# Performance work log

Measured on AMD Instinct MI355X. Metric: run time of the kernel, lower is better.

Reference implementation:

```python
import jax, jax.numpy as jnp
from jax import lax
import numpy as np

N_FFT = 256
HOP = 128
NUM_EXPERTS = 8
TOPK = 2
B = 128
L = 4096


def conv1d(x, w, b, pad):
    # x [N,C,T], w [O,I,K]
    y = lax.conv_general_dilated(x, w, (1,), [(pad, pad)],
                                 dimension_numbers=('NCH', 'OIH', 'NCH'))
    return y + b[None, :, None]


def maxpool1d(x, p):
    return lax.reduce_window(x, -jnp.inf, lax.max, (1, 1, p), (1, 1, p), 'VALID')


def se_block(x, w1, w2):
    # x [B,C,T]; squeeze-excitation with no-bias linears
    y = x.mean(-1)
    y = jax.nn.relu(y @ w1.T)
    y = jax.nn.sigmoid(y @ w2.T)
    return x * y[:, :, None]


def interp_linear(x, out_len):
    # F.interpolate(mode='linear', align_corners=False) on [B,C,T]
    Lin = x.shape[-1]
    scale = Lin / out_len
    coords = jnp.clip((jnp.arange(out_len, dtype=x.dtype) + 0.5) * scale - 0.5, 0.0, Lin - 1)
    lo = jnp.floor(coords).astype(jnp.int32)
    hi = jnp.minimum(lo + 1, Lin - 1)
    w = (coords - lo).astype(x.dtype)
    return x[..., lo] * (1.0 - w) + x[..., hi] * w


def lstm_scan(x, wih, whh, bih, bhh):
    # x [T,B,D] -> hidden seq [T,B,H]; torch gate order i,f,g,o
    H = whh.shape[1]
    def step(carry, xt):
        h, c = carry
        gates = xt @ wih.T + h @ whh.T + bih + bhh
        i, f, g, o = jnp.split(gates, 4, axis=-1)
        c = jax.nn.sigmoid(f) * c + jax.nn.sigmoid(i) * jnp.tanh(g)
        h = jax.nn.sigmoid(o) * jnp.tanh(c)
        return (h, c), h
    z = jnp.zeros((x.shape[1], H), x.dtype)
    _, hs = lax.scan(step, (z, z), x)
    return hs


def _forward(x_continuum, x_normalized,
             gate_w1, gate_b1, gate_w2, gate_b2,
             exp_w1, exp_b1, exp_w2, exp_b2,
             lw1, lb1, lw2, lb2, se2_w1, se2_w2, lw3, lb3, se3_w1, se3_w2,
             wih_f, whh_f, bih_f, bhh_f, wih_b, whh_b, bih_b, bhh_b,
             ffn_w1, ffn_b1, ffn_w2, ffn_b2):
    Bsz = x_continuum.shape[0]
    # --- STFT magnitude (center=True, reflect pad, periodic hann window) ---
    n = jnp.arange(N_FFT, dtype=x_continuum.dtype)
    win = 0.5 * (1.0 - jnp.cos(2.0 * jnp.pi * n / N_FFT))
    xp = jnp.pad(x_continuum, ((0, 0), (N_FFT // 2, N_FFT // 2)), mode='reflect')
    n_frames = 1 + (xp.shape[1] - N_FFT) // HOP  # 33
    idx = jnp.arange(n_frames)[:, None] * HOP + jnp.arange(N_FFT)[None, :]
    frames = xp[:, idx] * win                      # [B,T,N_FFT]
    mag = jnp.abs(jnp.fft.rfft(frames, axis=-1)).transpose(0, 2, 1)  # [B,129,T]
    mag = mag.astype(x_continuum.dtype)
    # --- gating: mean-pool over time, MLP, top-k, softmax over top-k ---
    pooled = mag.mean(-1)                          # [B,129]
    logits = jax.nn.relu(pooled @ gate_w1.T + gate_b1) @ gate_w2.T + gate_b2
    topv, topi = lax.top_k(logits, TOPK)
    gw = jax.nn.softmax(topv, axis=1)              # [B,K]
    # --- dense all-expert conv pyramids (matches original dense compute) ---
    def expert(w1, b1, w2, b2):
        h = jax.nn.relu(conv1d(mag, w1, b1, 2))
        return jax.nn.relu(conv1d(h, w2, b2, 1))
    eo = jax.vmap(expert)(exp_w1, exp_b1, exp_w2, exp_b2)  # [E,B,C,T]
    sel = eo[topi, jnp.arange(Bsz)[:, None]]               # [B,K,C,T]
    freq_feat = jnp.einsum('bk,bkct->bct', gw, sel)        # [B,256,33]
    # --- line attention branch ---
    h = jax.nn.relu(conv1d(x_normalized[:, None, :], lw1, lb1, 3))
    h = maxpool1d(h, 4)
    h = jax.nn.relu(conv1d(h, lw2, lb2, 2))
    h = se_block(h, se2_w1, se2_w2)
    h = maxpool1d(h, 4)
    h = jax.nn.relu(conv1d(h, lw3, lb3, 1))
    h = se_block(h, se3_w1, se3_w2)
    line_feat = maxpool1d(h, 4)                            # [B,256,64]
    # --- length alignment via linear interpolation ---
    t = min(freq_feat.shape[-1], line_feat.shape[-1])
    freq_feat = interp_linear(freq_feat, t)
    line_feat = interp_linear(line_feat, t)
    comb = jnp.concatenate([freq_feat, line_feat], axis=1).transpose(2, 0, 1)  # [T,B,512]
    # --- single-layer bidirectional LSTM, take last time step ---
    hf = lstm_scan(comb, wih_f, whh_f, bih_f, bhh_f)
    hb = lstm_scan(comb[::-1], wih_b, whh_b, bih_b, bhh_b)[::-1]
    last = jnp.concatenate([hf[-1], hb[-1]], axis=-1)      # [B,512]
    # --- prediction head (dropout inactive at inference) ---
    h = jax.nn.relu(last @ ffn_w1.T + ffn_b1)
    return h @ ffn_w2.T + ffn_b2                           # [B,1]


def setup_inputs() -> dict:
    key = jax.random.key(0)
    ks = jax.random.split(key, 40)
    def rn(k, shape, s=0.05):
        return jax.random.normal(k, shape, dtype=jnp.float32) * s
    d = {
        'x_continuum': jax.random.normal(ks[0], (B, L), jnp.float32),
        'x_normalized': jax.random.normal(ks[1], (B, L), jnp.float32),
        'gate_w1': rn(ks[2], (128, 129)), 'gate_b1': rn(ks[3], (128,)),
        'gate_w2': rn(ks[4], (NUM_EXPERTS, 128)), 'gate_b2': rn(ks[5], (NUM_EXPERTS,)),
        'exp_w1': rn(ks[6], (NUM_EXPERTS, 256, 129, 5)), 'exp_b1': rn(ks[7], (NUM_EXPERTS, 256)),
        'exp_w2': rn(ks[8], (NUM_EXPERTS, 256, 256, 3)), 'exp_b2': rn(ks[9], (NUM_EXPERTS, 256)),
        'lw1': rn(ks[10], (64, 1, 7)), 'lb1': rn(ks[11], (64,)),
        'lw2': rn(ks[12], (128, 64, 5)), 'lb2': rn(ks[13], (128,)),
        'se2_w1': rn(ks[14], (32, 128)), 'se2_w2': rn(ks[15], (128, 32)),
        'lw3': rn(ks[16], (256, 128, 3)), 'lb3': rn(ks[17], (256,)),
        'se3_w1': rn(ks[18], (64, 256)), 'se3_w2': rn(ks[19], (256, 64)),
        'wih_f': rn(ks[20], (1024, 512)), 'whh_f': rn(ks[21], (1024, 256)),
        'bih_f': rn(ks[22], (1024,)), 'bhh_f': rn(ks[23], (1024,)),
        'wih_b': rn(ks[24], (1024, 512)), 'whh_b': rn(ks[25], (1024, 256)),
        'bih_b': rn(ks[26], (1024,)), 'bhh_b': rn(ks[27], (1024,)),
        'ffn_w1': rn(ks[28], (256, 512)), 'ffn_b1': rn(ks[29], (256,)),
        'ffn_w2': rn(ks[30], (1, 256)), 'ffn_b2': rn(ks[31], (1,)),
    }
    return d


def reference(x_continuum, x_normalized,
              gate_w1, gate_b1, gate_w2, gate_b2,
              exp_w1, exp_b1, exp_w2, exp_b2,
              lw1, lb1, lw2, lb2, se2_w1, se2_w2, lw3, lb3, se3_w1, se3_w2,
              wih_f, whh_f, bih_f, bhh_f, wih_b, whh_b, bih_b, bhh_b,
              ffn_w1, ffn_b1, ffn_w2, ffn_b2):
    return _forward(x_continuum, x_normalized,
                    gate_w1, gate_b1, gate_w2, gate_b2,
                    exp_w1, exp_b1, exp_w2, exp_b2,
                    lw1, lb1, lw2, lb2, se2_w1, se2_w2, lw3, lb3, se3_w1, se3_w2,
                    wih_f, whh_f, bih_f, bhh_f, wih_b, whh_b, bih_b, bhh_b,
                    ffn_w1, ffn_b1, ffn_w2, ffn_b2)
```

## Files before the change

kernel.cpp:

```cpp
#include <hip/hip_runtime.h>
#include <math.h>

namespace {
constexpr int B = 128;
constexpr int L = 4096;
constexpr int NBIN = 129;
constexpr int NFR = 33;

constexpr size_t F_MAG    = 0;
constexpr size_t F_GW     = F_MAG + 544896;
constexpr size_t F_TOPI   = F_GW + 256;
constexpr size_t F_EH1    = F_TOPI + 256;
constexpr size_t F_SEL    = F_EH1 + 2162688;
constexpr size_t F_LINEF  = F_SEL + 2162688;
constexpr size_t F_COMB   = F_LINEF + 2097152;
constexpr size_t F_XPROJ  = F_COMB + 2162688;
constexpr size_t F_GATESB = F_XPROJ + 4325376;
constexpr size_t F_HF     = F_GATESB + 131072;
constexpr size_t F_HBLAST = F_HF + 32768;
constexpr size_t F_SESUM2 = F_HBLAST + 32768;
constexpr size_t F_SESC2  = F_SESUM2 + 16384;
constexpr size_t F_SESUM3 = F_SESC2 + 16384;
constexpr size_t F_SESC3  = F_SESUM3 + 32768;
constexpr size_t F_WHHB   = F_SESC3 + 32768;
constexpr size_t F_WKB    = F_WHHB + 131072;
constexpr size_t F_WKB3   = F_WKB + 20480;
constexpr size_t F_WIHF   = F_WKB3 + 49152;
constexpr size_t F_WIHB   = F_WIHF + 262144;
constexpr size_t F_BIGA   = F_WIHB + 262144;
constexpr size_t F_BIGB   = F_BIGA + 8388608;
}

typedef __attribute__((ext_vector_type(8))) short bf16x8;
typedef __attribute__((ext_vector_type(4))) float f32x4;

__device__ __forceinline__ float sigm(float x) { return 1.0f / (1.0f + expf(-x)); }

__device__ __forceinline__ float fsigm(float x) { return 1.0f / (1.0f + __expf(-x)); }
__device__ __forceinline__ float ftanh(float x) { return 1.0f - 2.0f / (__expf(2.0f * x) + 1.0f); }

__device__ __forceinline__ unsigned int f2bf_rne(float f) {
    unsigned int u = __float_as_uint(f);
    return (u + 0x7FFFu + ((u >> 16) & 1u)) >> 16;
}

__device__ __forceinline__ float bflo(unsigned int u) { return __uint_as_float(u << 16); }
__device__ __forceinline__ float bfhi(unsigned int u) { return __uint_as_float(u & 0xFFFF0000u); }

__global__ __launch_bounds__(256) void stft_kernel(const float* __restrict__ x,
                                                   float* __restrict__ mag)
{
    int bf = blockIdx.x;
    int b = bf / NFR, f = bf % NFR;
    int tid = threadIdx.x;
    __shared__ float tbl[256];
    __shared__ float fx[256];
    tbl[tid] = cosf(6.28318530717958647692f * (float)tid / 256.0f);
    __syncthreads();
    {
        int j = f * 128 + tid - 128;
        if (j < 0) j = -j;
        else if (j >= L) j = 2 * L - 2 - j;
        float win = 0.5f * (1.0f - tbl[tid]);
        fx[tid] = x[(size_t)b * L + j] * win;
    }
    __syncthreads();
    if (tid < NBIN) {
        float re = 0.f, im = 0.f;
        int m = 0;
        for (int n = 0; n < 256; ++n) {
            float v = fx[n];
            re += v * tbl[m];
            im += v * tbl[(m + 192) & 255];
            m = (m + tid) & 255;
        }
        mag[((size_t)b * NBIN + tid) * NFR + f] = sqrtf(re * re + im * im);
    }
}

__global__ __launch_bounds__(128) void gate_kernel(const float* __restrict__ mag,
                                                   const float* __restrict__ w1,
                                                   const float* __restrict__ b1,
                                                   const float* __restrict__ w2,
                                                   const float* __restrict__ b2,
                                                   int* __restrict__ topi,
                                                   float* __restrict__ gw)
{
    int b = blockIdx.x, tid = threadIdx.x;
    __shared__ float pooled[NBIN];
    __shared__ float h1[128];
    __shared__ float lg[8];
    for (int k = tid; k < NBIN; k += 128) {
        const float* mp = mag + ((size_t)b * NBIN + k) * NFR;
        float s = 0.f;
        for (int f = 0; f < NFR; ++f) s += mp[f];
        pooled[k] = s * (1.0f / 33.0f);
    }
    __syncthreads();
    {
        float acc = b1[tid];
        const float* wr = w1 + tid * NBIN;
        for (int k = 0; k < NBIN; ++k) acc += pooled[k] * wr[k];
        h1[tid] = fmaxf(acc, 0.f);
    }
    __syncthreads();
    if (tid < 8) {
        float a = b2[tid];
        const float* w = w2 + tid * 128;
        for (int j = 0; j < 128; ++j) a += h1[j] * w[j];
        lg[tid] = a;
    }
    __syncthreads();
    if (tid == 0) {
        int i0 = 0; float v0 = lg[0];
        for (int e = 1; e < 8; ++e) if (lg[e] > v0) { v0 = lg[e]; i0 = e; }
        int i1 = -1; float v1 = -3.0e38f;
        for (int e = 0; e < 8; ++e) { if (e == i0) continue; if (lg[e] > v1) { v1 = lg[e]; i1 = e; } }
        float m = fmaxf(v0, v1);
        float e0 = expf(v0 - m), e1 = expf(v1 - m);
        float inv = 1.0f / (e0 + e1);
        topi[b * 2 + 0] = i0; topi[b * 2 + 1] = i1;
        gw[b * 2 + 0] = e0 * inv; gw[b * 2 + 1] = e1 * inv;
    }
}

__global__ __launch_bounds__(512) void expert_conv1_kernel(const float* __restrict__ mag,
                                                           const int* __restrict__ topi,
                                                           const float* __restrict__ W,
                                                           const float* __restrict__ Bb,
                                                           float* __restrict__ out)
{
    int b = blockIdx.x, slot = blockIdx.y;
    int e = topi[b * 2 + slot];
    __shared__ float sm[129 * 37 + 16];
    int tid = threadIdx.x;
    for (int i = tid; i < 129 * 37 + 16; i += 512) sm[i] = 0.f;
    __syncthreads();
    for (int i = tid; i < 129 * 33; i += 512) {
        int ic = i / 33, t = i % 33;
        sm[ic * 37 + 2 + t] = mag[((size_t)b * NBIN + ic) * NFR + t];
    }
    __syncthreads();
    int oc = (blockIdx.z << 7) + (tid >> 2);
    int tq = tid & 3;
    int t0 = tq * 9;
    int nt = (tq == 3) ? 6 : 9;
    float acc[9];
#pragma unroll
    for (int i = 0; i < 9; ++i) acc[i] = 0.f;
    const float* wp = W + ((size_t)e * 256 + oc) * (129 * 5);
    for (int ic = 0; ic < 129; ++ic) {
        const float* wr = wp + ic * 5;
        const float* sr = sm + ic * 37 + t0;
        float w0 = wr[0], w1 = wr[1], w2 = wr[2], w3 = wr[3], w4 = wr[4];
#pragma unroll
        for (int t = 0; t < 9; ++t)
            acc[t] += w0 * sr[t] + w1 * sr[t + 1] + w2 * sr[t + 2] + w3 * sr[t + 3] + w4 * sr[t + 4];
    }
    float bias = Bb[e * 256 + oc];
    float* op = out + (((size_t)b * 2 + slot) * 256 + oc) * NFR + t0;
    for (int t = 0; t < nt; ++t) op[t] = fmaxf(acc[t] + bias, 0.f);
}

__global__ __launch_bounds__(512) void expert_conv2_kernel(const float* __restrict__ eh1,
                                                           const int* __restrict__ topi,
                                                           const float* __restrict__ W,
                                                           const float* __restrict__ Bb,
                                                           float* __restrict__ out)
{
    int b = blockIdx.x, slot = blockIdx.y;
    int e = topi[b * 2 + slot];
    __shared__ float sm[256 * 37 + 16];
    int tid = threadIdx.x;
    for (int i = tid; i < 256 * 37 + 16; i += 512) sm[i] = 0.f;
    __syncthreads();
    for (int i = tid; i < 256 * 33; i += 512) {
        int ic = i / 33, t = i % 33;
        sm[ic * 37 + 2 + t] = eh1[(((size_t)b * 2 + slot) * 256 + ic) * NFR + t];
    }
    __syncthreads();
    int oc = (blockIdx.z << 7) + (tid >> 2);
    int tq = tid & 3;
    int t0 = tq * 9;
    int nt = (tq == 3) ? 6 : 9;
    float acc[9];
#pragma unroll
    for (int i = 0; i < 9; ++i) acc[i] = 0.f;
    const float* wp = W + ((size_t)e * 256 + oc) * (256 * 3);
    for (int ic = 0; ic < 256; ++ic) {
        const float* wr = wp + ic * 3;
        const float* sr = sm + ic * 37 + t0;
        float w0 = wr[0], w1 = wr[1], w2 = wr[2];
#pragma unroll
        for (int t = 0; t < 9; ++t)
            acc[t] += w0 * sr[t + 1] + w1 * sr[t + 2] + w2 * sr[t + 3];
    }
    float bias = Bb[e * 256 + oc];
    float* op = out + (((size_t)b * 2 + slot) * 256 + oc) * NFR + t0;
    for (int t = 0; t < nt; ++t) op[t] = fmaxf(acc[t] + bias, 0.f);
}

__global__ __launch_bounds__(256) void line1_kernel(const float* __restrict__ x,
                                                    const float* __restrict__ lw1,
                                                    const float* __restrict__ lb1,
                                                    unsigned short* __restrict__ p1T)
{
    int b = blockIdx.x;
    int P0 = blockIdx.y * 256;
    __shared__ float sx[1032];
    __shared__ float w[448];
    __shared__ float bb[64];
    __shared__ unsigned short sT[256 * 65];
    int tid = threadIdx.x;
    for (int i = tid; i < 448; i += 256) w[i] = lw1[i];
    for (int i = tid; i < 64; i += 256) bb[i] = lb1[i];
    int base = 4 * P0 - 3;
    for (int i = tid; i < 1032; i += 256) {
        int g = base + i;
        sx[i] = (g >= 0 && g < L) ? x[(size_t)b * L + g] : 0.f;
    }
    __syncthreads();
    int p = tid;
    for (int oc = 0; oc < 64; ++oc) {
        const float* wr = w + oc * 7;
        float best = -3.0e38f;
#pragma unroll
        for (int q = 0; q < 4; ++q) {
            const float* s = sx + 4 * p + q;
            float v = wr[0]*s[0] + wr[1]*s[1] + wr[2]*s[2] + wr[3]*s[3] + wr[4]*s[4] + wr[5]*s[5] + wr[6]*s[6];
            best = fmaxf(best, v);
        }
        float v = fmaxf(best + bb[oc], 0.f);
        sT[p * 65 + oc] = (unsigned short)f2bf_rne(v);
    }
    __syncthreads();
    unsigned int* outw = reinterpret_cast<unsigned int*>(p1T);
    for (int i2 = tid; i2 < 256 * 32; i2 += 256) {
        int row = i2 >> 5, dw = i2 & 31;
        unsigned int lo = sT[row * 65 + dw * 2];
        unsigned int hi = sT[row * 65 + dw * 2 + 1];
        outw[((size_t)b * 1024 + P0 + row) * 32 + dw] = lo | (hi << 16);
    }
}

__global__ __launch_bounds__(256) void prep_wkb_kernel(const float* __restrict__ W,
                                                       unsigned short* __restrict__ wkb)
{
    int idx = blockIdx.x * 256 + threadIdx.x;
    if (idx >= 128 * 320) return;
    int oc = idx / 320, K = idx % 320;
    int k = K >> 6, ic = K & 63;
    wkb[idx] = (unsigned short)f2bf_rne(W[oc * 320 + ic * 5 + k]);
}

__global__ __launch_bounds__(256) void line2_mfma_kernel(const unsigned short* __restrict__ p1T,
                                                         const unsigned short* __restrict__ wkb,
                                                         const float* __restrict__ lb2,
                                                         float* __restrict__ h2,
                                                         float* __restrict__ seSum2)
{
    int b = blockIdx.x;
    int t0 = blockIdx.y * 128;
    __shared__ __align__(16) unsigned short wl[128 * 320];
    __shared__ __align__(16) unsigned short inT[132 * 64];
    __shared__ float bias[128];
    int tid = threadIdx.x;

    for (int idx = tid; idx < 128 * 40; idx += 256) {
        int oc = idx / 40, ch = idx % 40;
        int swz = (ch & ~7) | ((ch & 7) ^ (oc & 7));
        *reinterpret_cast<uint4*>(&wl[oc * 320 + swz * 8]) =
            *reinterpret_cast<const uint4*>(&wkb[oc * 320 + ch * 8]);
    }
    for (int idx = tid; idx < 132 * 8; idx += 256) {
        int j = idx / 8, ch = idx % 8;
        int t = t0 - 2 + j;
        uint4 v = make_uint4(0u, 0u, 0u, 0u);
        if (t >= 0 && t < 1024)
            v = *reinterpret_cast<const uint4*>(&p1T[((size_t)b * 1024 + t) * 64 + ch * 8]);
        int swz = ch ^ (j & 7);
        *reinterpret_cast<uint4*>(&inT[j * 64 + swz * 8]) = v;
    }
    if (tid < 128) bias[tid] = lb2[tid];
    __syncthreads();

    int lane = tid & 63;
    int w = tid >> 6;
    int l15 = lane & 15, g = lane >> 4;

    f32x4 acc[8][2];
#pragma unroll
    for (int ot = 0; ot < 8; ++ot) {
        acc[ot][0] = (f32x4){0.f, 0.f, 0.f, 0.f};
        acc[ot][1] = (f32x4){0.f, 0.f, 0.f, 0.f};
    }

    for (int ks = 0; ks < 10; ++ks) {
        int k = ks >> 1;
        bf16x8 bf0, bf1;
        {
            int j = w * 32 + l15 + k;
            int ch = (ks & 1) * 4 + g;
            bf0 = *reinterpret_cast<const bf16x8*>(&inT[j * 64 + (ch ^ (j & 7)) * 8]);
            int j1 = j + 16;
            bf1 = *reinterpret_cast<const bf16x8*>(&inT[j1 * 64 + (ch ^ (j1 & 7)) * 8]);
        }
#pragma unroll
        for (int ot = 0; ot < 8; ++ot) {
            int row = ot * 16 + l15;
            int ch = ks * 4 + g;
            int swz = (ch & ~7) | ((ch & 7) ^ (row & 7));
            bf16x8 af = *reinterpret_cast<const bf16x8*>(&wl[row * 320 + swz * 8]);
            acc[ot][0] = __builtin_amdgcn_mfma_f32_16x16x32_bf16(af, bf0, acc[ot][0], 0, 0, 0);
            acc[ot][1] = __builtin_amdgcn_mfma_f32_16x16x32_bf16(af, bf1, acc[ot][1], 0, 0, 0);
        }
    }

    int tcol = t0 + w * 32 + l15;
#pragma unroll
    for (int ot = 0; ot < 8; ++ot) {
#pragma unroll
        for (int r = 0; r < 4; ++r) {
            int oc = ot * 16 + g * 4 + r;
            float bv = bias[oc];
            float v0 = fmaxf(acc[ot][0][r] + bv, 0.f);
            float v1 = fmaxf(acc[ot][1][r] + bv, 0.f);
            float* hp = h2 + ((size_t)b * 128 + oc) * 1024 + tcol;
            hp[0] = v0;
            hp[16] = v1;
            float s = v0 + v1;
            s += __shfl_xor(s, 1);
            s += __shfl_xor(s, 2);
            s += __shfl_xor(s, 4);
            s += __shfl_xor(s, 8);
            if (l15 == 0) atomicAdd(&seSum2[b * 128 + oc], s);
        }
    }
}

__global__ __launch_bounds__(128) void se2_kernel(const float* __restrict__ seSum2,
                                                  const float* __restrict__ w1,
                                                  const float* __restrict__ w2,
                                                  float* __restrict__ seScale2)
{
    int b = blockIdx.x, tid = threadIdx.x;
    __shared__ float y[128];
    __shared__ float z[32];
    y[tid] = seSum2[b * 128 + tid] * (1.0f / 1024.0f);
    __syncthreads();
    if (tid < 32) {
        float a = 0.f;
        const float* wr = w1 + tid * 128;
        for (int c = 0; c < 128; ++c) a += y[c] * wr[c];
        z[tid] = fmaxf(a, 0.f);
    }
    __syncthreads();
    {
        float a = 0.f;
        const float* wr = w2 + tid * 32;
        for (int j = 0; j < 32; ++j) a += z[j] * wr[j];
        seScale2[b * 128 + tid] = sigm(a);
    }
}

__global__ __launch_bounds__(256) void pool2t_kernel(const float* __restrict__ h2,
                                                     const float* __restrict__ seScale2,
                                                     unsigned short* __restrict__ p2T)
{
    int b = blockIdx.x, p = threadIdx.x;
    __shared__ unsigned short sT[256 * 129];
    for (int c = 0; c < 128; ++c) {
        float4 v = *reinterpret_cast<const float4*>(&h2[((size_t)b * 128 + c) * 1024 + 4 * p]);
        float m = fmaxf(fmaxf(v.x, v.y), fmaxf(v.z, v.w)) * seScale2[b * 128 + c];
        sT[p * 129 + c] = (unsigned short)f2bf_rne(m);
    }
    __syncthreads();
    unsigned int* out = reinterpret_cast<unsigned int*>(p2T);
    for (int idx = p; idx < 256 * 64; idx += 256) {
        int row = idx >> 6, dw = idx & 63;
        unsigned int lo = sT[row * 129 + dw * 2];
        unsigned int hi = sT[row * 129 + dw * 2 + 1];
        out[((size_t)b * 256 + row) * 64 + dw] = lo | (hi << 16);
    }
}

__global__ __launch_bounds__(256) void prep_wkb3_kernel(const float* __restrict__ W,
                                                        unsigned short* __restrict__ wkb3)
{
    int idx = blockIdx.x * 256 + threadIdx.x;
    if (idx >= 256 * 384) return;
    int oc = idx / 384, K = idx % 384;
    int k = K >> 7, ic = K & 127;
    wkb3[idx] = (unsigned short)f2bf_rne(W[oc * 384 + ic * 3 + k]);
}

__global__ __launch_bounds__(256) void line3_mfma_kernel(const unsigned short* __restrict__ p2T,
                                                         const unsigned short* __restrict__ wkb3,
                                                         const float* __restrict__ lb3,
                                                         float* __restrict__ h3,
                                                         float* __restrict__ seSum3)
{
    int b = blockIdx.x;
    int oc0 = blockIdx.y * 128;
    int t0 = blockIdx.z * 128;
    __shared__ __align__(16) unsigned short wl[128 * 384];
    __shared__ __align__(16) unsigned short inT[130 * 128];
    __shared__ float bias[128];
    int tid = threadIdx.x;

    for (int idx = tid; idx < 128 * 48; idx += 256) {
        int oc = idx / 48, ch = idx % 48;
        int swz = (ch & ~7) | ((ch & 7) ^ (oc & 7));
        *reinterpret_cast<uint4*>(&wl[oc * 384 + swz * 8]) =
            *reinterpret_cast<const uint4*>(&wkb3[(size_t)(oc0 + oc) * 384 + ch * 8]);
    }
    for (int idx = tid; idx < 130 * 16; idx += 256) {
        int j = idx / 16, ch = idx % 16;
        int t = t0 - 1 + j;
        uint4 v = make_uint4(0u, 0u, 0u, 0u);
        if (t >= 0 && t < 256)
            v = *reinterpret_cast<const uint4*>(&p2T[((size_t)b * 256 + t) * 128 + ch * 8]);
        int swz = ch ^ (j & 15);
        *reinterpret_cast<uint4*>(&inT[j * 128 + swz * 8]) = v;
    }
    if (tid < 128) bias[tid] = lb3[oc0 + tid];
    __syncthreads();

    int lane = tid & 63;
    int w = tid >> 6;
    int l15 = lane & 15, g = lane >> 4;

    f32x4 acc[8][2];
#pragma unroll
    for (int ot = 0; ot < 8; ++ot) {
        acc[ot][0] = (f32x4){0.f, 0.f, 0.f, 0.f};
        acc[ot][1] = (f32x4){0.f, 0.f, 0.f, 0.f};
    }

    for (int ks = 0; ks < 12; ++ks) {
        int k = ks >> 2;
        int ch = (ks & 3) * 4 + g;
        bf16x8 bf0, bf1;
        {
            int j = w * 32 + l15 + k;
            bf0 = *reinterpret_cast<const bf16x8*>(&inT[j * 128 + (ch ^ (j & 15)) * 8]);
            int j1 = j + 16;
            bf1 = *reinterpret_cast<const bf16x8*>(&inT[j1 * 128 + (ch ^ (j1 & 15)) * 8]);
        }
#pragma unroll
        for (int ot = 0; ot < 8; ++ot) {
            int row = ot * 16 + l15;
            int wch = ks * 4 + g;
            int swz = (wch & ~7) | ((wch & 7) ^ (row & 7));
            bf16x8 af = *reinterpret_cast<const bf16x8*>(&wl[row * 384 + swz * 8]);
            acc[ot][0] = __builtin_amdgcn_mfma_f32_16x16x32_bf16(af, bf0, acc[ot][0], 0, 0, 0);
            acc[ot][1] = __builtin_amdgcn_mfma_f32_16x16x32_bf16(af, bf1, acc[ot][1], 0, 0, 0);
        }
    }

    int tcol = t0 + w * 32 + l15;
#pragma unroll
    for (int ot = 0; ot < 8; ++ot) {
#pragma unroll
        for (int r = 0; r < 4; ++r) {
            int ocl = ot * 16 + g * 4 + r;
            int oc = oc0 + ocl;
            float bv = bias[ocl];
            float v0 = fmaxf(acc[ot][0][r] + bv, 0.f);
            float v1 = fmaxf(acc[ot][1][r] + bv, 0.f);
            float* hp = h3 + ((size_t)b * 256 + oc) * 256 + tcol;
            hp[0] = v0;
            hp[16] = v1;
            float s = v0 + v1;
            s += __shfl_xor(s, 1);
            s += __shfl_xor(s, 2);
            s += __shfl_xor(s, 4);
            s += __shfl_xor(s, 8);
            if (l15 == 0) atomicAdd(&seSum3[b * 256 + oc], s);
        }
    }
}

__global__ __launch_bounds__(256) void se3_kernel(const float* __restrict__ seSum3,
                                                  const float* __restrict__ w1,
                                                  const float* __restrict__ w2,
                                                  float* __restrict__ seScale3)
{
    int b = blockIdx.x, tid = threadIdx.x;
    __shared__ float y[256];
    __shared__ float z[64];
    y[tid] = seSum3[b * 256 + tid] * (1.0f / 256.0f);
    __syncthreads();
    if (tid < 64) {
        float a = 0.f;
        const float* wr = w1 + tid * 256;
        for (int c = 0; c < 256; ++c) a += y[c] * wr[c];
        z[tid] = fmaxf(a, 0.f);
    }
    __syncthreads();
    {
        float a = 0.f;
        const float* wr = w2 + tid * 64;
        for (int j = 0; j < 64; ++j) a += z[j] * wr[j];
        seScale3[b * 256 + tid] = sigm(a);
    }
}

__global__ __launch_bounds__(256) void pool3_kernel(const float* __restrict__ h3,
                                                    const float* __restrict__ seScale3,
                                                    float* __restrict__ lineFeat)
{
    const int total = 128 * 256 * 64;
    for (int idx = blockIdx.x * 256 + threadIdx.x; idx < total; idx += gridDim.x * 256) {
        int b = idx >> 14;
        int c = (idx >> 6) & 255;
        int p = idx & 63;
        const float* hp = h3 + (((size_t)b * 256 + c) * 256) + 4 * p;
        float v = fmaxf(fmaxf(hp[0], hp[1]), fmaxf(hp[2], hp[3]));
        lineFeat[idx] = v * seScale3[b * 256 + c];
    }
}

__global__ __launch_bounds__(256) void comb_kernel(const float* __restrict__ sel,
                                                   const float* __restrict__ gw,
                                                   const float* __restrict__ lineFeat,
                                                   unsigned short* __restrict__ combB)
{
    const int total = 33 * 128 * 512;
    for (int idx = blockIdx.x * 256 + threadIdx.x; idx < total; idx += gridDim.x * 256) {
        int c = idx & 511;
        int r = idx >> 9;
        int b = r & 127;
        int t = r >> 7;
        float v;
        if (c < 256) {
            float g0 = gw[b * 2 + 0], g1 = gw[b * 2 + 1];
            v = g0 * sel[(((size_t)b * 2 + 0) * 256 + c) * NFR + t]
              + g1 * sel[(((size_t)b * 2 + 1) * 256 + c) * NFR + t];
        } else {
            int cc = c - 256;
            float xc = ((float)t + 0.5f) * (64.0f / 33.0f) - 0.5f;
            xc = fminf(fmaxf(xc, 0.0f), 63.0f);
            int lo = (int)floorf(xc);
            int hi = lo + 1; if (hi > 63) hi = 63;
            float w = xc - (float)lo;
            const float* lp = lineFeat + ((size_t)b * 256 + cc) * 64;
            v = lp[lo] * (1.0f - w) + lp[hi] * w;
        }
        combB[idx] = (unsigned short)f2bf_rne(v);
    }
}

__global__ __launch_bounds__(256) void pack_bf16_kernel(const float* __restrict__ in,
                                                        unsigned short* __restrict__ out,
                                                        int n)
{
    int i = (blockIdx.x * 256 + threadIdx.x) * 4;
    if (i >= n) return;
    float4 v = *reinterpret_cast<const float4*>(in + i);
    uint2 w;
    w.x = f2bf_rne(v.x) | (f2bf_rne(v.y) << 16);
    w.y = f2bf_rne(v.z) | (f2bf_rne(v.w) << 16);
    *reinterpret_cast<uint2*>(out + i) = w;
}

__global__ __launch_bounds__(256) void gemm_mfma_kernel(const unsigned short* __restrict__ A,
                                                        const unsigned short* __restrict__ W,
                                                        const float* __restrict__ b1,
                                                        const float* __restrict__ b2,
                                                        float* __restrict__ out)
{
    int row0 = blockIdx.x * 128;
    int col0 = blockIdx.y * 128;
    __shared__ __align__(16) unsigned short As[128 * 64];
    __shared__ __align__(16) unsigned short Bs[128 * 64];
    __shared__ float bias[128];
    int tid = threadIdx.x;
    if (tid < 128) bias[tid] = b1[col0 + tid] + b2[col0 + tid];
    int lane = tid & 63, w = tid >> 6, l15 = lane & 15, g = lane >> 4;

    f32x4 acc[8][2];
#pragma unroll
    for (int ot = 0; ot < 8; ++ot) {
        acc[ot][0] = (f32x4){0.f, 0.f, 0.f, 0.f};
        acc[ot][1] = (f32x4){0.f, 0.f, 0.f, 0.f};
    }

    for (int kc = 0; kc < 8; ++kc) {
        __syncthreads();
        for (int idx = tid; idx < 1024; idx += 256) {
            int r = idx >> 3, ch = idx & 7;
            int swz = ch ^ (r & 7);
            *reinterpret_cast<uint4*>(&As[r * 64 + swz * 8]) =
                *reinterpret_cast<const uint4*>(&A[(size_t)(row0 + r) * 512 + kc * 64 + ch * 8]);
            *reinterpret_cast<uint4*>(&Bs[r * 64 + swz * 8]) =
                *reinterpret_cast<const uint4*>(&W[(size_t)(col0 + r) * 512 + kc * 64 + ch * 8]);
        }
        __syncthreads();
#pragma unroll
        for (int ks = 0; ks < 2; ++ks) {
            int ch = ks * 4 + g;
            int j = w * 32 + l15;
            bf16x8 bf0 = *reinterpret_cast<const bf16x8*>(&As[j * 64 + (ch ^ (j & 7)) * 8]);
            int j1 = j + 16;
            bf16x8 bf1 = *reinterpret_cast<const bf16x8*>(&As[j1 * 64 + (ch ^ (j1 & 7)) * 8]);
#pragma unroll
            for (int ot = 0; ot < 8; ++ot) {
                int row = ot * 16 + l15;
                bf16x8 af = *reinterpret_cast<const bf16x8*>(&Bs[row * 64 + (ch ^ (row & 7)) * 8]);
                acc[ot][0] = __builtin_amdgcn_mfma_f32_16x16x32_bf16(af, bf0, acc[ot][0], 0, 0, 0);
                acc[ot][1] = __builtin_amdgcn_mfma_f32_16x16x32_bf16(af, bf1, acc[ot][1], 0, 0, 0);
            }
        }
    }

    int rbase = row0 + w * 32 + l15;
#pragma unroll
    for (int ot = 0; ot < 8; ++ot) {
#pragma unroll
        for (int r = 0; r < 4; ++r) {
            int ocl = ot * 16 + g * 4 + r;
            float bv = bias[ocl];
            out[(size_t)rbase * 1024 + col0 + ocl] = acc[ot][0][r] + bv;
            out[(size_t)(rbase + 16) * 1024 + col0 + ocl] = acc[ot][1][r] + bv;
        }
    }
}

__global__ __launch_bounds__(256) void prep_whh4_kernel(const float* __restrict__ W,
                                                        uint4* __restrict__ whh4)
{
    int idx = blockIdx.x * 256 + threadIdx.x;
    int k8 = idx >> 10, j = idx & 1023;
    const float* src = W + (size_t)j * 256 + k8 * 8;
    float4 v0 = *reinterpret_cast<const float4*>(src);
    float4 v1 = *reinterpret_cast<const float4*>(src + 4);
    uint4 w;
    w.x = f2bf_rne(v0.x) | (f2bf_rne(v0.y) << 16);
    w.y = f2bf_rne(v0.z) | (f2bf_rne(v0.w) << 16);
    w.z = f2bf_rne(v1.x) | (f2bf_rne(v1.y) << 16);
    w.w = f2bf_rne(v1.z) | (f2bf_rne(v1.w) << 16);
    whh4[(size_t)k8 * 1024 + j] = w;
}

__global__ __launch_bounds__(1024) void lstm_fused_kernel(const float* __restrict__ xproj,
                                                          const uint4* __restrict__ whh4,
                                                          float* __restrict__ hfinal)
{
    int b = blockIdx.x;
    int j = threadIdx.x;
    __shared__ __align__(16) float h[256];
    __shared__ float cc[256];
    __shared__ float g[1024];
    if (j < 256) { h[j] = 0.f; cc[j] = 0.f; }
    __syncthreads();
    const uint4* wp = whh4 + j;
    for (int t = 0; t < 33; ++t) {
        float a0 = xproj[(size_t)t * 131072 + (size_t)b * 1024 + j];
        float a1 = 0.f;
#pragma unroll 8
        for (int k8 = 0; k8 < 32; ++k8) {
            uint4 w = wp[k8 << 10];
            float4 h0 = *reinterpret_cast<const float4*>(&h[k8 * 8]);
            float4 h1 = *reinterpret_cast<const float4*>(&h[k8 * 8 + 4]);
            a0 += bflo(w.x) * h0.x + bfhi(w.x) * h0.y + bflo(w.y) * h0.z + bfhi(w.y) * h0.w;
            a1 += bflo(w.z) * h1.x + bfhi(w.z) * h1.y + bflo(w.w) * h1.z + bfhi(w.w) * h1.w;
        }
        g[j] = a0 + a1;
        __syncthreads();
        if (j < 256) {
            float gi = g[j], gf = g[256 + j], gz = g[512 + j], go = g[768 + j];
            float c = fsigm(gf) * cc[j] + fsigm(gi) * ftanh(gz);
            cc[j] = c;
            h[j] = fsigm(go) * ftanh(c);
        }
        __syncthreads();
    }
    if (j < 256) hfinal[b * 256 + j] = h[j];
}

__global__ __launch_bounds__(256) void lstm_bwd_tail_kernel(const float* __restrict__ gatesB,
                                                            float* __restrict__ hbLast)
{
    int b = blockIdx.x, u = threadIdx.x;
    const float* g = gatesB + (size_t)b * 1024;
    float ai = g[u], ag = g[512 + u], ao = g[768 + u];
    float c = sigm(ai) * tanhf(ag);
    hbLast[b * 256 + u] = sigm(ao) * tanhf(c);
}

__global__ __launch_bounds__(256) void ffn_kernel(const float* __restrict__ hf,
                                                  const float* __restrict__ hb,
                                                  const float* __restrict__ w1,
                                                  const float* __restrict__ b1,
                                                  const float* __restrict__ w2,
                                                  const float* __restrict__ b2,
                                                  float* __restrict__ out)
{
    int b = blockIdx.x, tid = threadIdx.x;
    __shared__ float last[512];
    __shared__ float red[256];
    last[tid] = hf[b * 256 + tid];
    last[256 + tid] = hb[b * 256 + tid];
    __syncthreads();
    float a = b1[tid];
    const float* wr = w1 + (size_t)tid * 512;
    for (int k = 0; k < 512; ++k) a += last[k] * wr[k];
    red[tid] = fmaxf(a, 0.f) * w2[tid];
    __syncthreads();
    for (int s = 128; s > 0; s >>= 1) {
        if (tid < s) red[tid] += red[tid + s];
        __syncthreads();
    }
    if (tid == 0) out[b] = red[0] + b2[0];
}

extern "C" void kernel_launch(void* const* d_in, const int* in_sizes, int n_in,
                              void* d_out, int out_size, void* d_ws, size_t ws_size,
                              hipStream_t stream)
{
    (void)in_sizes; (void)n_in; (void)out_size; (void)ws_size;
    const float* x_cont = (const float*)d_in[0];
    const float* x_norm = (const float*)d_in[1];
    const float* gate_w1 = (const float*)d_in[2];
    const float* gate_b1 = (const float*)d_in[3];
    const float* gate_w2 = (const float*)d_in[4];
    const float* gate_b2 = (const float*)d_in[5];
    const float* exp_w1 = (const float*)d_in[6];
    const float* exp_b1 = (const float*)d_in[7];
    const float* exp_w2 = (const float*)d_in[8];
    const float* exp_b2 = (const float*)d_in[9];
    const float* lw1 = (const float*)d_in[10];
    const float* lb1 = (const float*)d_in[11];
    const float* lw2 = (const float*)d_in[12];
    const float* lb2 = (const float*)d_in[13];
    const float* se2_w1 = (const float*)d_in[14];
    const float* se2_w2 = (const float*)d_in[15];
    const float* lw3 = (const float*)d_in[16];
    const float* lb3 = (const float*)d_in[17];
    const float* se3_w1 = (const float*)d_in[18];
    const float* se3_w2 = (const float*)d_in[19];
    const float* wih_f = (const float*)d_in[20];
    const float* whh_f = (const float*)d_in[21];
    const float* bih_f = (const float*)d_in[22];
    const float* bhh_f = (const float*)d_in[23];
    const float* wih_b = (const float*)d_in[24];
    const float* whh_b = (const float*)d_in[25];
    const float* bih_b = (const float*)d_in[26];
    const float* bhh_b = (const float*)d_in[27];
    const float* ffn_w1 = (const float*)d_in[28];
    const float* ffn_b1 = (const float*)d_in[29];
    const float* ffn_w2 = (const float*)d_in[30];
    const float* ffn_b2 = (const float*)d_in[31];

    float* ws = (float*)d_ws;
    float* mag     = ws + F_MAG;
    float* gw      = ws + F_GW;
    int*   topi    = (int*)(ws + F_TOPI);
    float* eh1     = ws + F_EH1;
    float* sel     = ws + F_SEL;
    float* lineFeat= ws + F_LINEF;
    unsigned short* combB = (unsigned short*)(ws + F_COMB);
    float* xproj   = ws + F_XPROJ;
    float* gatesB  = ws + F_GATESB;
    float* hfF     = ws + F_HF;
    float* hbLast  = ws + F_HBLAST;
    float* seSum2  = ws + F_SESUM2;
    float* seSc2   = ws + F_SESC2;
    float* seSum3  = ws + F_SESUM3;
    float* seSc3   = ws + F_SESC3;
    uint4* whh4    = (uint4*)(ws + F_WHHB);
    unsigned short* wkb  = (unsigned short*)(ws + F_WKB);
    unsigned short* wkb3 = (unsigned short*)(ws + F_WKB3);
    unsigned short* wihFb = (unsigned short*)(ws + F_WIHF);
    unsigned short* wihBb = (unsigned short*)(ws + F_WIHB);
    unsigned short* p1T = (unsigned short*)(ws + F_BIGA);
    float* h2      = ws + F_BIGB;
    unsigned short* p2T = (unsigned short*)(ws + F_BIGA);
    float* h3      = ws + F_BIGB;

    hipMemsetAsync(seSum2, 0, 16384 * sizeof(float), stream);
    hipMemsetAsync(seSum3, 0, 32768 * sizeof(float), stream);

    stft_kernel<<<B * NFR, 256, 0, stream>>>(x_cont, mag);
    gate_kernel<<<B, 128, 0, stream>>>(mag, gate_w1, gate_b1, gate_w2, gate_b2, topi, gw);
    expert_conv1_kernel<<<dim3(B, 2, 2), 512, 0, stream>>>(mag, topi, exp_w1, exp_b1, eh1);
    expert_conv2_kernel<<<dim3(B, 2, 2), 512, 0, stream>>>(eh1, topi, exp_w2, exp_b2, sel);

    prep_wkb_kernel<<<160, 256, 0, stream>>>(lw2, wkb);
    line1_kernel<<<dim3(B, 4), 256, 0, stream>>>(x_norm, lw1, lb1, p1T);
    line2_mfma_kernel<<<dim3(B, 8), 256, 0, stream>>>(p1T, wkb, lb2, h2, seSum2);
    se2_kernel<<<B, 128, 0, stream>>>(seSum2, se2_w1, se2_w2, seSc2);
    pool2t_kernel<<<B, 256, 0, stream>>>(h2, seSc2, p2T);
    prep_wkb3_kernel<<<384, 256, 0, stream>>>(lw3, wkb3);
    line3_mfma_kernel<<<dim3(B, 2, 2), 256, 0, stream>>>(p2T, wkb3, lb3, h3, seSum3);
    se3_kernel<<<B, 256, 0, stream>>>(seSum3, se3_w1, se3_w2, seSc3);
    pool3_kernel<<<2048, 256, 0, stream>>>(h3, seSc3, lineFeat);

    comb_kernel<<<2048, 256, 0, stream>>>(sel, gw, lineFeat, combB);

    pack_bf16_kernel<<<512, 256, 0, stream>>>(wih_f, wihFb, 1024 * 512);
    pack_bf16_kernel<<<512, 256, 0, stream>>>(wih_b, wihBb, 1024 * 512);

    gemm_mfma_kernel<<<dim3(33, 8), 256, 0, stream>>>(combB, wihFb, bih_f, bhh_f, xproj);
    gemm_mfma_kernel<<<dim3(1, 8), 256, 0, stream>>>(combB + (size_t)4096 * 512, wihBb, bih_b, bhh_b, gatesB);
    lstm_bwd_tail_kernel<<<B, 256, 0, stream>>>(gatesB, hbLast);

    prep_whh4_kernel<<<128, 256, 0, stream>>>(whh_f, whh4);
    lstm_fused_kernel<<<B, 1024, 0, stream>>>(xproj, whh4, hfF);

    ffn_kernel<<<B, 256, 0, stream>>>(hfF, hbLast, ffn_w1, ffn_b1, ffn_w2, ffn_b2, (float*)d_out);
}
```

Baseline: 644.9 us.

## Rewrite expert conv1/conv2 as bf16 MFMA implicit GEMMs with prepacked weights

The two expert convolutions are recast as implicit GEMMs on bf16 MFMA instructions. The STFT now also writes a time-major bf16 copy of the magnitude, expert weights are repacked into a k-major bf16 layout, and the conv1 output is kept as bf16 in time-major layout for conv2. The goal is to move the dominant scalar FP32 FMA work onto matrix cores, using swizzled LDS tiles to avoid bank conflicts. The cost is two extra weight-packing kernels per call, large LDS tiles that reduce occupancy, and bf16 rounding error in the expert path.

```diff
diff --git a/kernel.cpp b/kernel.cpp
--- a/kernel.cpp
+++ b/kernel.cpp
@@ -29,13 +29,15 @@
 constexpr size_t F_WIHB   = F_WIHF + 262144;
 constexpr size_t F_BIGA   = F_WIHB + 262144;
 constexpr size_t F_BIGB   = F_BIGA + 8388608;
+constexpr size_t A_WKBE1  = F_XPROJ;
+constexpr size_t A_WKBE2  = F_XPROJ + 720896;
+constexpr size_t A_MAGT   = F_XPROJ + 1507328;
 }
 
 typedef __attribute__((ext_vector_type(8))) short bf16x8;
 typedef __attribute__((ext_vector_type(4))) float f32x4;
 
 __device__ __forceinline__ float sigm(float x) { return 1.0f / (1.0f + expf(-x)); }
-
 __device__ __forceinline__ float fsigm(float x) { return 1.0f / (1.0f + __expf(-x)); }
 __device__ __forceinline__ float ftanh(float x) { return 1.0f - 2.0f / (__expf(2.0f * x) + 1.0f); }
 
@@ -43,12 +45,12 @@
     unsigned int u = __float_as_uint(f);
     return (u + 0x7FFFu + ((u >> 16) & 1u)) >> 16;
 }
-
 __device__ __forceinline__ float bflo(unsigned int u) { return __uint_as_float(u << 16); }
 __device__ __forceinline__ float bfhi(unsigned int u) { return __uint_as_float(u & 0xFFFF0000u); }
 
 __global__ __launch_bounds__(256) void stft_kernel(const float* __restrict__ x,
-                                                   float* __restrict__ mag)
+                                                   float* __restrict__ mag,
+                                                   unsigned short* __restrict__ magT)
 {
     int bf = blockIdx.x;
     int b = bf / NFR, f = bf % NFR;
@@ -74,7 +76,11 @@
             im += v * tbl[(m + 192) & 255];
             m = (m + tid) & 255;
         }
-        mag[((size_t)b * NBIN + tid) * NFR + f] = sqrtf(re * re + im * im);
+        float val = sqrtf(re * re + im * im);
+        mag[((size_t)b * NBIN + tid) * NFR + f] = val;
+        magT[((size_t)b * NFR + f) * 136 + tid] = (unsigned short)f2bf_rne(val);
+    } else if (tid < 136) {
+        magT[((size_t)b * NFR + f) * 136 + tid] = 0;
     }
 }
 
@@ -124,80 +130,155 @@
     }
 }
 
-__global__ __launch_bounds__(512) void expert_conv1_kernel(const float* __restrict__ mag,
-                                                           const int* __restrict__ topi,
-                                                           const float* __restrict__ W,
-                                                           const float* __restrict__ Bb,
-                                                           float* __restrict__ out)
-{
-    int b = blockIdx.x, slot = blockIdx.y;
+__global__ __launch_bounds__(256) void prep_wkbE1_kernel(const float* __restrict__ W,
+                                                         unsigned short* __restrict__ out)
+{
+    int idx = blockIdx.x * 256 + threadIdx.x;
+    if (idx >= 8 * 256 * 704) return;
+    int eo = idx / 704, K = idx % 704;
+    int k = K / 136, ic = K - k * 136;
+    float v = (k < 5 && ic < 129) ? W[((size_t)eo * 129 + ic) * 5 + k] : 0.f;
+    out[idx] = (unsigned short)f2bf_rne(v);
+}
+
+__global__ __launch_bounds__(256) void prep_wkbE2_kernel(const float* __restrict__ W,
+                                                         unsigned short* __restrict__ out)
+{
+    int idx = blockIdx.x * 256 + threadIdx.x;
+    if (idx >= 8 * 256 * 768) return;
+    int eo = idx / 768, K = idx % 768;
+    int k = K >> 8, ic = K & 255;
+    out[idx] = (unsigned short)f2bf_rne(W[((size_t)eo * 256 + ic) * 3 + k]);
+}
+
+__global__ __launch_bounds__(256) void expert_conv1_mfma(const unsigned short* __restrict__ magT,
+                                                         const int* __restrict__ topi,
+                                                         const unsigned short* __restrict__ wkbE1,
+                                                         const float* __restrict__ Bb,
+                                                         unsigned short* __restrict__ eh1T)
+{
+    int b = blockIdx.x, slot = blockIdx.y, ocq = blockIdx.z;
     int e = topi[b * 2 + slot];
-    __shared__ float sm[129 * 37 + 16];
+    __shared__ __align__(16) unsigned short wl[64 * 704];
+    __shared__ __align__(16) unsigned short inT[37 * 136];
+    __shared__ float bias[64];
     int tid = threadIdx.x;
-    for (int i = tid; i < 129 * 37 + 16; i += 512) sm[i] = 0.f;
-    __syncthreads();
-    for (int i = tid; i < 129 * 33; i += 512) {
-        int ic = i / 33, t = i % 33;
-        sm[ic * 37 + 2 + t] = mag[((size_t)b * NBIN + ic) * NFR + t];
-    }
-    __syncthreads();
-    int oc = (blockIdx.z << 7) + (tid >> 2);
-    int tq = tid & 3;
-    int t0 = tq * 9;
-    int nt = (tq == 3) ? 6 : 9;
-    float acc[9];
-#pragma unroll
-    for (int i = 0; i < 9; ++i) acc[i] = 0.f;
-    const float* wp = W + ((size_t)e * 256 + oc) * (129 * 5);
-    for (int ic = 0; ic < 129; ++ic) {
-        const float* wr = wp + ic * 5;
-        const float* sr = sm + ic * 37 + t0;
-        float w0 = wr[0], w1 = wr[1], w2 = wr[2], w3 = wr[3], w4 = wr[4];
-#pragma unroll
-        for (int t = 0; t < 9; ++t)
-            acc[t] += w0 * sr[t] + w1 * sr[t + 1] + w2 * sr[t + 2] + w3 * sr[t + 3] + w4 * sr[t + 4];
-    }
-    float bias = Bb[e * 256 + oc];
-    float* op = out + (((size_t)b * 2 + slot) * 256 + oc) * NFR + t0;
-    for (int t = 0; t < nt; ++t) op[t] = fmaxf(acc[t] + bias, 0.f);
-}
-
-__global__ __launch_bounds__(512) void expert_conv2_kernel(const float* __restrict__ eh1,
-                                                           const int* __restrict__ topi,
-                                                           const float* __restrict__ W,
-                                                           const float* __restrict__ Bb,
-                                                           float* __restrict__ out)
-{
-    int b = blockIdx.x, slot = blockIdx.y;
+    for (int idx = tid; idx < 64 * 88; idx += 256) {
+        int oc = idx / 88, ch = idx % 88;
+        int swz = (ch & ~7) | ((ch & 7) ^ (oc & 7));
+        *reinterpret_cast<uint4*>(&wl[oc * 704 + swz * 8]) =
+            *reinterpret_cast<const uint4*>(&wkbE1[((size_t)(e * 256 + ocq * 64 + oc)) * 704 + ch * 8]);
+    }
+    for (int idx = tid; idx < 37 * 17; idx += 256) {
+        int j = idx / 17, ch = idx % 17;
+        int tp = j - 2;
+        uint4 v = make_uint4(0u, 0u, 0u, 0u);
+        if (tp >= 0 && tp < 33)
+            v = *reinterpret_cast<const uint4*>(&magT[((size_t)b * NFR + tp) * 136 + ch * 8]);
+        *reinterpret_cast<uint4*>(&inT[j * 136 + ch * 8]) = v;
+    }
+    if (tid < 64) bias[tid] = Bb[e * 256 + ocq * 64 + tid];
+    __syncthreads();
+
+    int lane = tid & 63, w = tid >> 6, l15 = lane & 15, g = lane >> 4;
+    f32x4 acc[3];
+#pragma unroll
+    for (int n = 0; n < 3; ++n) acc[n] = (f32x4){0.f, 0.f, 0.f, 0.f};
+
+    int row = w * 16 + l15;
+    for (int ks = 0; ks < 22; ++ks) {
+        int ch = ks * 4 + g;
+        bf16x8 af = *reinterpret_cast<const bf16x8*>(
+            &wl[row * 704 + (((ch & ~7) | ((ch & 7) ^ (row & 7)))) * 8]);
+        int ce = ch > 84 ? 84 : ch;
+        int k = ce / 17, icc = ce - k * 17;
+#pragma unroll
+        for (int n = 0; n < 3; ++n) {
+            int t = n * 16 + l15;
+            int j = t + k; if (j > 36) j = 36;
+            bf16x8 bf = *reinterpret_cast<const bf16x8*>(&inT[j * 136 + icc * 8]);
+            acc[n] = __builtin_amdgcn_mfma_f32_16x16x32_bf16(af, bf, acc[n], 0, 0, 0);
+        }
+    }
+#pragma unroll
+    for (int n = 0; n < 3; ++n) {
+        int t = n * 16 + l15;
+        if (t < 33) {
+            float v0 = fmaxf(acc[n][0] + bias[w * 16 + g * 4 + 0], 0.f);
+            float v1 = fmaxf(acc[n][1] + bias[w * 16 + g * 4 + 1], 0.f);
+            float v2 = fmaxf(acc[n][2] + bias[w * 16 + g * 4 + 2], 0.f);
+            float v3 = fmaxf(acc[n][3] + bias[w * 16 + g * 4 + 3], 0.f);
+            uint2 pk;
+            pk.x = f2bf_rne(v0) | (f2bf_rne(v1) << 16);
+            pk.y = f2bf_rne(v2) | (f2bf_rne(v3) << 16);
+            *reinterpret_cast<uint2*>(
+                &eh1T[(((size_t)(b * 2 + slot)) * NFR + t) * 256 + ocq * 64 + w * 16 + g * 4]) = pk;
+        }
+    }
+}
+
+__global__ __launch_bounds__(256) void expert_conv2_mfma(const unsigned short* __restrict__ eh1T,
+                                                         const int* __restrict__ topi,
+                                                         const unsigned short* __restrict__ wkbE2,
+                                                         const float* __restrict__ Bb,
+                                                         float* __restrict__ sel)
+{
+    int b = blockIdx.x, slot = blockIdx.y, ocq = blockIdx.z;
     int e = topi[b * 2 + slot];
-    __shared__ float sm[256 * 37 + 16];
+    __shared__ __align__(16) unsigned short wl[64 * 768];
+    __shared__ __align__(16) unsigned short inT[35 * 256];
+    __shared__ float bias[64];
     int tid = threadIdx.x;
-    for (int i = tid; i < 256 * 37 + 16; i += 512) sm[i] = 0.f;
-    __syncthreads();
-    for (int i = tid; i < 256 * 33; i += 512) {
-        int ic = i / 33, t = i % 33;
-        sm[ic * 37 + 2 + t] = eh1[(((size_t)b * 2 + slot) * 256 + ic) * NFR + t];
-    }
-    __syncthreads();
-    int oc = (blockIdx.z << 7) + (tid >> 2);
-    int tq = tid & 3;
-    int t0 = tq * 9;
-    int nt = (tq == 3) ? 6 : 9;
-    float acc[9];
-#pragma unroll
-    for (int i = 0; i < 9; ++i) acc[i] = 0.f;
-    const float* wp = W + ((size_t)e * 256 + oc) * (256 * 3);
-    for (int ic = 0; ic < 256; ++ic) {
-        const float* wr = wp + ic * 3;
-        const float* sr = sm + ic * 37 + t0;
-        float w0 = wr[0], w1 = wr[1], w2 = wr[2];
-#pragma unroll
-        for (int t = 0; t < 9; ++t)
-            acc[t] += w0 * sr[t + 1] + w1 * sr[t + 2] + w2 * sr[t + 3];
-    }
-    float bias = Bb[e * 256 + oc];
-    float* op = out + (((size_t)b * 2 + slot) * 256 + oc) * NFR + t0;
-    for (int t = 0; t < nt; ++t) op[t] = fmaxf(acc[t] + bias, 0.f);
+    for (int idx = tid; idx < 64 * 96; idx += 256) {
+        int oc = idx / 96, ch = idx % 96;
+        int swz = (ch & ~7) | ((ch & 7) ^ (oc & 7));
+        *reinterpret_cast<uint4*>(&wl[oc * 768 + swz * 8]) =
+            *reinterpret_cast<const uint4*>(&wkbE2[((size_t)(e * 256 + ocq * 64 + oc)) * 768 + ch * 8]);
+    }
+    for (int idx = tid; idx < 35 * 32; idx += 256) {
+        int j = idx / 32, ch = idx % 32;
+        int tp = j - 1;
+        uint4 v = make_uint4(0u, 0u, 0u, 0u);
+        if (tp >= 0 && tp < 33)
+            v = *reinterpret_cast<const uint4*>(&eh1T[(((size_t)(b * 2 + slot)) * NFR + tp) * 256 + ch * 8]);
+        int swz = (ch & ~15) | ((ch & 15) ^ (j & 15));
+        *reinterpret_cast<uint4*>(&inT[j * 256 + swz * 8]) = v;
+    }
+    if (tid < 64) bias[tid] = Bb[e * 256 + ocq * 64 + tid];
+    __syncthreads();
+
+    int lane = tid & 63, w = tid >> 6, l15 = lane & 15, g = lane >> 4;
+    f32x4 acc[3];
+#pragma unroll
+    for (int n = 0; n < 3; ++n) acc[n] = (f32x4){0.f, 0.f, 0.f, 0.f};
+
+    int row = w * 16 + l15;
+    for (int ks = 0; ks < 24; ++ks) {
+        int ch = ks * 4 + g;
+        bf16x8 af = *reinterpret_cast<const bf16x8*>(
+            &wl[row * 768 + (((ch & ~7) | ((ch & 7) ^ (row & 7)))) * 8]);
+        int k = ch >> 5, icc = ch & 31;
+#pragma unroll
+        for (int n = 0; n < 3; ++n) {
+            int t = n * 16 + l15;
+            int j = t + k; if (j > 34) j = 34;
+            int sz = (icc & ~15) | ((icc & 15) ^ (j & 15));
+            bf16x8 bf = *reinterpret_cast<const bf16x8*>(&inT[j * 256 + sz * 8]);
+            acc[n] = __builtin_amdgcn_mfma_f32_16x16x32_bf16(af, bf, acc[n], 0, 0, 0);
+        }
+    }
+#pragma unroll
+    for (int n = 0; n < 3; ++n) {
+        int t = n * 16 + l15;
+        if (t < 33) {
+#pragma unroll
+            for (int r = 0; r < 4; ++r) {
+                int oc = ocq * 64 + w * 16 + g * 4 + r;
+                float v = fmaxf(acc[n][r] + bias[w * 16 + g * 4 + r], 0.f);
+                sel[(((size_t)b * 2 + slot) * 256 + oc) * NFR + t] = v;
+            }
+        }
+    }
 }
 
 __global__ __launch_bounds__(256) void line1_kernel(const float* __restrict__ x,
@@ -757,7 +838,7 @@
     float* mag     = ws + F_MAG;
     float* gw      = ws + F_GW;
     int*   topi    = (int*)(ws + F_TOPI);
-    float* eh1     = ws + F_EH1;
+    unsigned short* eh1T = (unsigned short*)(ws + F_EH1);
     float* sel     = ws + F_SEL;
     float* lineFeat= ws + F_LINEF;
     unsigned short* combB = (unsigned short*)(ws + F_COMB);
@@ -774,6 +855,9 @@
     unsigned short* wkb3 = (unsigned short*)(ws + F_WKB3);
     unsigned short* wihFb = (unsigned short*)(ws + F_WIHF);
     unsigned short* wihBb = (unsigned short*)(ws + F_WIHB);
+    unsigned short* wkbE1 = (unsigned short*)(ws + A_WKBE1);
+    unsigned short* wkbE2 = (unsigned short*)(ws + A_WKBE2);
+    unsigned short* magT  = (unsigned short*)(ws + A_MAGT);
     unsigned short* p1T = (unsigned short*)(ws + F_BIGA);
     float* h2      = ws + F_BIGB;
     unsigned short* p2T = (unsigned short*)(ws + F_BIGA);
@@ -782,10 +866,13 @@
     hipMemsetAsync(seSum2, 0, 16384 * sizeof(float), stream);
     hipMemsetAsync(seSum3, 0, 32768 * sizeof(float), stream);
 
-    stft_kernel<<<B * NFR, 256, 0, stream>>>(x_cont, mag);
+    prep_wkbE1_kernel<<<5632, 256, 0, stream>>>(exp_w1, wkbE1);
+    prep_wkbE2_kernel<<<6144, 256, 0, stream>>>(exp_w2, wkbE2);
+
+    stft_kernel<<<B * NFR, 256, 0, stream>>>(x_cont, mag, magT);
     gate_kernel<<<B, 128, 0, stream>>>(mag, gate_w1, gate_b1, gate_w2, gate_b2, topi, gw);
-    expert_conv1_kernel<<<dim3(B, 2, 2), 512, 0, stream>>>(mag, topi, exp_w1, exp_b1, eh1);
-    expert_conv2_kernel<<<dim3(B, 2, 2), 512, 0, stream>>>(eh1, topi, exp_w2, exp_b2, sel);
+    expert_conv1_mfma<<<dim3(B, 2, 4), 256, 0, stream>>>(magT, topi, wkbE1, exp_b1, eh1T);
+    expert_conv2_mfma<<<dim3(B, 2, 4), 256, 0, stream>>>(eh1T, topi, wkbE2, exp_b2, sel);
 
     prep_wkb_kernel<<<160, 256, 0, stream>>>(lw2, wkb);
     line1_kernel<<<dim3(B, 4), 256, 0, stream>>>(x_norm, lw1, lb1, p1T);
```

New measurement: 591.7 us. 1.09x faster.
